# Kernel tuning notes

Measured on AMD Instinct MI355X. Metric: run time of the kernel, lower is better.

The kernel has to match this reference:

```python
import jax, jax.numpy as jnp
import numpy as np

IN_CH = 8      # in_channels
CIN = 80       # cin_channels (mel)
DI_BASE = 2
POS_GROUP = 4
NCH = 256      # n_channels
NLAYERS = 8
K = 3          # kernel_size
B = 1          # spect batch; audio batch = B * POS_GROUP
T = 4096
C2L = 2 * NCH * NLAYERS


def _conv1x1(x, w, b):
    # x: [B, C, T], w: [O, C], b: [O]
    return jnp.einsum('bct,oc->bot', x, w) + b[None, :, None]


def _dilated_conv(x, w, b, dilation):
    # x: [B, C, T], w: [O, C, K], 'same' padding as in torch Conv1d
    pad = dilation * (K - 1) // 2
    y = jax.lax.conv_general_dilated(
        x, w, window_strides=(1,), padding=[(pad, pad)],
        rhs_dilation=(dilation,), dimension_numbers=('NCH', 'OIH', 'NCH'))
    return y + b[None, :, None]


def setup_inputs() -> dict:
    key = jax.random.key(0)
    ks = jax.random.split(key, 12)
    s = 0.05
    d = {}
    d['audio'] = jax.random.normal(ks[0], (B * POS_GROUP, IN_CH, T), jnp.float32)
    d['spect'] = jax.random.normal(ks[1], (B, CIN, T), jnp.float32)
    d['pos'] = jax.random.randint(ks[2], (B * POS_GROUP,), 0, POS_GROUP)
    d['start_w'] = jax.random.normal(ks[3], (NCH, IN_CH), jnp.float32) * s
    d['start_b'] = jnp.zeros((NCH,), jnp.float32)
    d['cond_w'] = jax.random.normal(ks[4], (C2L, CIN), jnp.float32) * s
    d['cond_b'] = jnp.zeros((C2L,), jnp.float32)
    d['pos_emb_w'] = jax.random.normal(ks[5], (POS_GROUP, 128), jnp.float32) * s
    d['pos_lin_w'] = jax.random.normal(ks[6], (C2L, 128), jnp.float32) * s
    d['pos_lin_b'] = jnp.zeros((C2L,), jnp.float32)
    d['in_w'] = jax.random.normal(ks[7], (NLAYERS, 2 * NCH, NCH, K), jnp.float32) * s
    d['in_b'] = jnp.zeros((NLAYERS, 2 * NCH), jnp.float32)
    d['rs_w'] = jax.random.normal(ks[8], (NLAYERS - 1, 2 * NCH, NCH), jnp.float32) * s
    d['rs_b'] = jnp.zeros((NLAYERS - 1, 2 * NCH), jnp.float32)
    d['rs_last_w'] = jax.random.normal(ks[9], (NCH, NCH), jnp.float32) * s
    d['rs_last_b'] = jnp.zeros((NCH,), jnp.float32)
    d['end_w'] = jax.random.normal(ks[10], (2 * IN_CH, NCH), jnp.float32) * s
    d['end_b'] = jnp.zeros((2 * IN_CH,), jnp.float32)
    return d


def reference(audio, spect, pos, start_w, start_b, cond_w, cond_b,
              pos_emb_w, pos_lin_w, pos_lin_b, in_w, in_b,
              rs_w, rs_b, rs_last_w, rs_last_b, end_w, end_b):
    h = _conv1x1(audio, start_w, start_b)               # [BG, NCH, T]
    out = jnp.zeros_like(h)
    cond = _conv1x1(spect, cond_w, cond_b)              # [B, 2*NCH*L, T]
    # repeat(1, pos_group, 1).view(-1, C, T) == consecutive batch tiling
    cond = jnp.repeat(cond, POS_GROUP, axis=0)          # [BG, 2*NCH*L, T]
    pe = jax.nn.relu(pos_emb_w[pos])                    # [BG, 128]
    pc = (pe @ pos_lin_w.T + pos_lin_b)[:, :, None]     # [BG, 2*NCH*L, 1]
    for i in range(NLAYERS):
        off = i * 2 * NCH
        in_act = (_dilated_conv(h, in_w[i], in_b[i], DI_BASE ** i)
                  + cond[:, off:off + 2 * NCH]
                  + pc[:, off:off + 2 * NCH])
        acts = jnp.tanh(in_act[:, :NCH]) * jax.nn.sigmoid(in_act[:, NCH:])
        if i < NLAYERS - 1:
            rs = _conv1x1(acts, rs_w[i], rs_b[i])       # [BG, 2*NCH, T]
            h = h + rs[:, :NCH]
            out = out + rs[:, NCH:]
        else:
            out = out + _conv1x1(acts, rs_last_w, rs_last_b)
    y = _conv1x1(out, end_w, end_b)                     # [BG, 2*IN_CH, T]
    return y[:, :IN_CH], y[:, IN_CH:]
```

## Files before the change

kernel.cpp:

```cpp
#include <hip/hip_runtime.h>
#include <stdint.h>

#define T_LEN 4096
#define PAD   128
#define HROWS (T_LEN + 2*PAD)
#define NCH   256
#define M2    512
#define BG    4
#define NL    8

using f4  = __attribute__((ext_vector_type(4))) float;
using bh8 = __attribute__((ext_vector_type(8))) short;
using s4v = __attribute__((ext_vector_type(4))) short;
using u4  = __attribute__((ext_vector_type(4))) unsigned int;

static __device__ __forceinline__ short f2b(float f){
  unsigned u = __builtin_bit_cast(unsigned, f);
  unsigned r = (u + 0x7FFFu + ((u >> 16) & 1u)) >> 16;
  return (short)r;
}
static __device__ __forceinline__ float b2f(short s){
  unsigned u = ((unsigned)(unsigned short)s) << 16;
  return __builtin_bit_cast(float, u);
}

#define MFMA(a,b,c) __builtin_amdgcn_mfma_f32_16x16x32_bf16((a),(b),(c),0,0,0)


#define PAD_BLK0 1024
#define E_BLK0   1280
#define ST_BLK0  1408
#define CB_BLK0  1536
#define H0_BLK0  1600
#define ALL_BLKS 1856

__global__ __launch_bounds__(256) void prep_all(
    const float* __restrict__ audio, const float* __restrict__ spect,
    const int* __restrict__ pos, const float* __restrict__ start_w,
    const float* __restrict__ start_b, const float* __restrict__ cond_w,
    const float* __restrict__ cond_b, const float* __restrict__ pos_emb_w,
    const float* __restrict__ pos_lin_w, const float* __restrict__ pos_lin_b,
    const float* __restrict__ in_w, const float* __restrict__ in_b,
    const float* __restrict__ rs_w, const float* __restrict__ rs_b,
    const float* __restrict__ rs_last_w, const float* __restrict__ rs_last_b,
    const float* __restrict__ end_w, const float* __restrict__ end_b,
    short* __restrict__ W1, short* __restrict__ W2, short* __restrict__ Wcn,
    float* __restrict__ rsb8, short* __restrict__ hA, short* __restrict__ hB,
    short* __restrict__ Es, float* __restrict__ ebl, short* __restrict__ spectT,
    float* __restrict__ cb){
  __shared__ float smem[4224];
  const int bid = blockIdx.x, tid = threadIdx.x;

  if (bid < PAD_BLK0){
    const int G1 = NL*3*8*8*4*64;
    const int G2 = NL*8*8*2*64;
    const int G4 = NL*8*4*4*64;
    const int n3 = NL*M2;
    for (int q = bid*256 + tid; q < G1+G2+G4+n3; q += 1024*256){
      if (q < G1){
        int lane = q & 63, f = (q >> 6) & 3, kk = (q >> 8) & 7, w = (q >> 11) & 7;
        int lt = q >> 14;
        int tap = lt % 3, l = lt / 3;
        int o = (f < 2) ? (w*32 + f*16 + (lane & 15)) : (256 + w*32 + (f-2)*16 + (lane & 15));
        int c0 = kk*32 + (lane >> 4)*8;
        const float* src = in_w + (((size_t)(l*M2 + o)*NCH + c0)*3) + tap;
        bh8 pk;
        #pragma unroll
        for (int j = 0; j < 8; ++j) pk[j] = f2b(src[j*3]);
        *(bh8*)(W1 + (size_t)q*8) = pk;
      } else if (q < G1+G2){
        int p = q - G1;
        int lane = p & 63, f = (p >> 6) & 1, kk = (p >> 7) & 7, w = (p >> 10) & 7;
        int l = p >> 13;
        int o = w*32 + f*16 + (lane & 15);
        int c0 = kk*32 + (lane >> 4)*8;
        bh8 pk;
        if (l < 7){
          const f4* s = (const f4*)(rs_w + ((size_t)(l*M2 + o))*NCH + c0);
          f4 a = s[0], bvv = s[1];
          #pragma unroll
          for (int j = 0; j < 4; ++j){ pk[j] = f2b(a[j]); pk[4+j] = f2b(bvv[j]); }
        } else {
          #pragma unroll
          for (int j = 0; j < 8; ++j) pk[j] = 0;
        }
        *(bh8*)(W2 + (size_t)p*8) = pk;
      } else if (q < G1+G2+G4){
        int p = q - G1 - G2;
        int lane = p & 63, f = (p >> 6) & 3, kk = (p >> 8) & 3, w = (p >> 10) & 7;
        int l = p >> 13;
        int o = (f < 2) ? (w*32 + f*16 + (lane & 15)) : (256 + w*32 + (f-2)*16 + (lane & 15));
        int k0 = kk*32 + (lane >> 4)*8;
        bh8 pk;
        if (k0 < 80){
          const f4* s = (const f4*)(cond_w + (size_t)(l*M2 + o)*80 + k0);
          f4 a = s[0], bvv = s[1];
          #pragma unroll
          for (int j = 0; j < 4; ++j){ pk[j] = f2b(a[j]); pk[4+j] = f2b(bvv[j]); }
        } else {
          #pragma unroll
          for (int j = 0; j < 8; ++j) pk[j] = 0;
        }
        *(bh8*)(Wcn + (size_t)p*8) = pk;
      } else {
        int k = q - G1 - G2 - G4;
        int o = k & 511, l = k >> 9;
        rsb8[k] = (l < 7) ? rs_b[l*M2 + o] : 0.f;
      }
    }
  } else if (bid < E_BLK0){
    int i = (bid - PAD_BLK0)*256 + tid;
    short* h = (i < 32768) ? hA : hB;
    int j = (i & 32767) << 3;
    int b = j >> 16;
    int r = j & 65535;
    int row = r >> 8, c = r & 255;
    int grow = (row < PAD) ? row : (T_LEN + PAD + (row - PAD));
    *(u4*)(h + ((size_t)b*HROWS + grow)*NCH + c) = (u4){0,0,0,0};
  } else if (bid < ST_BLK0){
    float* ew_s = smem; float* red = smem + 256;
    int e = bid - E_BLK0;
    const int l = e >> 4, o = e & 15;
    const int c = tid;
    ew_s[c] = end_w[o*256 + c];
    __syncthreads();
    const float* Wsrc = (l < 7) ? (rs_w + ((size_t)(l*M2 + NCH))*NCH) : rs_last_w;
    float acc = 0.f;
    #pragma unroll 8
    for (int cp = 0; cp < 256; ++cp)
      acc += ew_s[cp] * Wsrc[(size_t)cp*NCH + c];
    int kk = c >> 5, g = (c >> 3) & 3, j = c & 7;
    Es[(((size_t)l*8 + kk)*64 + g*16 + o)*8 + j] = f2b(acc);
    float bv = (l < 7) ? rs_b[l*M2 + NCH + c] : rs_last_b[c];
    red[c] = ew_s[c] * bv;
    __syncthreads();
    for (int s = 128; s > 0; s >>= 1){
      if (c < s) red[c] += red[c + s];
      __syncthreads();
    }
    if (c == 0) ebl[l*16 + o] = red[0] + ((l == 0) ? end_b[o] : 0.f);
  } else if (bid < CB_BLK0){
    float (*tile)[65] = (float(*)[65])smem;
    int e = bid - ST_BLK0;
    int t0 = (e & 63)*64, k0 = (e >> 6)*64;
    for (int i = tid; i < 64*64; i += 256){
      int kr = i >> 6, tt = i & 63;
      int k = k0 + kr;
      tile[kr][tt] = (k < 80) ? spect[(size_t)k*T_LEN + t0 + tt] : 0.f;
    }
    __syncthreads();
    for (int i = tid; i < 64*64; i += 256){
      int r = i >> 6, kk = i & 63;
      spectT[(size_t)(t0 + r)*128 + k0 + kk] = f2b(tile[kk][r]);
    }
  } else if (bid < H0_BLK0){
    int e = bid - CB_BLK0;
    int b = e >> 4;
    int ch = (e & 15)*256 + tid;
    int p = pos[b];
    float acc = pos_lin_b[ch] + in_b[ch] + cond_b[ch];
    for (int k = 0; k < 128; ++k){
      float ev = pos_emb_w[p*128 + k];
      ev = ev > 0.f ? ev : 0.f;
      acc += ev * pos_lin_w[ch*128 + k];
    }
    cb[b*4096 + ch] = acc;
  } else {
    float* sw = smem; float* sb = smem + 2048;
    int e = bid - H0_BLK0;
    int b = e >> 6, t0 = (e & 63)*64;
    for (int i = tid; i < NCH*8; i += 256) sw[i] = start_w[i];
    for (int i = tid; i < NCH;   i += 256) sb[i] = start_b[i];
    __syncthreads();
    int t = t0 + (tid & 63);
    int cg = tid >> 6;
    float av[8];
    #pragma unroll
    for (int ic = 0; ic < 8; ++ic) av[ic] = audio[((size_t)(b*8 + ic))*T_LEN + t];
    short* dst = hA + ((size_t)b*HROWS + PAD + t)*NCH;
    for (int c = cg*64; c < cg*64 + 64; ++c){
      float acc = sb[c];
      #pragma unroll
      for (int ic = 0; ic < 8; ++ic) acc += sw[c*8 + ic]*av[ic];
      dst[c] = f2b(acc);
    }
  }
}

template<int DIL>
__global__ __launch_bounds__(512, 2) void wn_layer(
    const short* __restrict__ hSrc, short* __restrict__ hDst,
    const short* __restrict__ W1l, const short* __restrict__ W2l,
    const short* __restrict__ Wcl, const short* __restrict__ Esl,
    const short* __restrict__ spectTp,
    const float* __restrict__ cb_l, const float* __restrict__ rsb_l,
    const float* __restrict__ ebl_l, float* __restrict__ yacc,
    int flags){

  __shared__ short Ht[192*NCH];
  __shared__ short xb[64*NCH];
  __shared__ short St[64*128];

  constexpr int tbR   = (DIL <= 64) ? DIL : 64;
  constexpr int WROWS = (DIL <= 64) ? (64 + 2*DIL) : 192;

  const int tid  = threadIdx.x;
  const int w    = tid >> 6, lane = tid & 63;
  const int l15  = lane & 15, g = lane >> 4;
  const int lin  = blockIdx.x + (blockIdx.y << 6);
  const int nl2  = ((lin & 7) << 5) + (lin >> 3);
  const int tile = nl2 & 63, b = nl2 >> 6;
  const int sw8  = (l15 & 7) << 3;
  const bool first = flags & 1, last = flags & 2;

  f4 acc[4][4];
  #pragma unroll
  for (int f = 0; f < 4; ++f)
    #pragma unroll
    for (int nf = 0; nf < 4; ++nf) acc[f][nf] = (f4){0.f,0.f,0.f,0.f};

  bh8 Ap[3][4], Bp[3][4];

#define LAc(S, BUF) do{ const short* _p = Wcl + w*8192 + (S)*2048 + lane*8; \
    Ap[BUF][0]=*(const bh8*)(_p);      Ap[BUF][1]=*(const bh8*)(_p+512); \
    Ap[BUF][2]=*(const bh8*)(_p+1024); Ap[BUF][3]=*(const bh8*)(_p+1536); }while(0)
#define LBc(S, BUF) do{ const int _c=((S)*32+g*8)^sw8; \
    Bp[BUF][0]=*(const bh8*)(St + ( 0+l15)*128 + _c); \
    Bp[BUF][1]=*(const bh8*)(St + (16+l15)*128 + _c); \
    Bp[BUF][2]=*(const bh8*)(St + (32+l15)*128 + _c); \
    Bp[BUF][3]=*(const bh8*)(St + (48+l15)*128 + _c); }while(0)
#define LA1(S, BUF) do{ const int _tap=(S)>>3, _kk=(S)&7; \
    const short* _p = W1l + _tap*131072 + w*16384 + _kk*2048 + lane*8; \
    Ap[BUF][0]=*(const bh8*)(_p);      Ap[BUF][1]=*(const bh8*)(_p+512); \
    Ap[BUF][2]=*(const bh8*)(_p+1024); Ap[BUF][3]=*(const bh8*)(_p+1536); }while(0)
#define LB1(S, BUF) do{ const int _tap=(S)>>3, _kk=(S)&7; \
    const int _tb=_tap*tbR; const int _sw=(((_tb+l15)&7)<<3); \
    const short* _hb = Ht + (_tb+l15)*NCH + ((_kk*32+g*8)^_sw); \
    Bp[BUF][0]=*(const bh8*)(_hb); \
    Bp[BUF][1]=*(const bh8*)(_hb + 16*NCH); \
    Bp[BUF][2]=*(const bh8*)(_hb + 32*NCH); \
    Bp[BUF][3]=*(const bh8*)(_hb + 48*NCH); }while(0)
#define LAX(S, BUF) do{ if((S)<3) LAc((S),BUF); else LA1((S)-3,BUF); }while(0)
#define LBX(S, BUF) do{ if((S)<3) LBc((S),BUF); else LB1((S)-3,BUF); }while(0)
#define LA2(S, BUF) do{ \
    const short* _p = W2l + w*8192 + (S)*1024 + lane*8; \
    Ap[BUF][0]=*(const bh8*)(_p);      Ap[BUF][1]=*(const bh8*)(_p+512); }while(0)
#define LB2(S, BUF) do{ const int _c=((S)*32+g*8)^sw8; \
    Bp[BUF][0]=*(const bh8*)(xb + ( 0+l15)*NCH + _c); \
    Bp[BUF][1]=*(const bh8*)(xb + (16+l15)*NCH + _c); \
    Bp[BUF][2]=*(const bh8*)(xb + (32+l15)*NCH + _c); \
    Bp[BUF][3]=*(const bh8*)(xb + (48+l15)*NCH + _c); }while(0)

  LAX(0, 0);

  {
    constexpr int SEGS = WROWS/2;
    #pragma unroll
    for (int k = 0; k < (SEGS + 7)/8; ++k){
      int seg = w + k*8;
      if (SEGS % 8 == 0 || seg < SEGS){
        int r = seg*2 + (lane >> 5);
        int grow = (DIL <= 64) ? (tile*64 - DIL + r)
                               : (tile*64 + ((r >> 6) - 1)*128 + (r & 63));
        int cb = ((lane & 31) << 4) ^ ((r & 7) << 4);
        const short* gp = hSrc + ((size_t)(b*HROWS + PAD + grow))*NCH + (cb >> 1);
        __builtin_amdgcn_global_load_lds(
            (const __attribute__((address_space(1))) unsigned int*)gp,
            (__attribute__((address_space(3))) unsigned int*)(Ht + seg*512),
            16, 0, 0);
      }
    }
    #pragma unroll
    for (int k = 0; k < 2; ++k){
      int seg = w + k*8;
      int r = seg*4 + (lane >> 4);
      int cb = ((lane & 15) << 4) ^ ((r & 7) << 4);
      const short* gp = spectTp + (size_t)(tile*64 + r)*128 + (cb >> 1);
      __builtin_amdgcn_global_load_lds(
          (const __attribute__((address_space(1))) unsigned int*)gp,
          (__attribute__((address_space(3))) unsigned int*)(St + seg*512),
          16, 0, 0);
    }
  }
  LAX(1, 1);
  __syncthreads();

  LBX(0, 0);
  LBX(1, 1);
  #pragma unroll
  for (int s = 0; s < 27; ++s){
    const int cur = s % 3, pf = (s+2) % 3;
    if (s < 25){ LAX(s+2, pf); LBX(s+2, pf); }
    #pragma unroll
    for (int f = 0; f < 4; ++f)
      #pragma unroll
      for (int nf = 0; nf < 4; ++nf)
        acc[f][nf] = MFMA(Ap[cur][f], Bp[cur][nf], acc[f][nf]);
  }

  float bias[4][4];
  #pragma unroll
  for (int f = 0; f < 4; ++f){
    int ch = ((f < 2) ? (w*32 + f*16) : (256 + w*32 + (f-2)*16)) + 4*g;
    f4 t = *(const f4*)(cb_l + b*4096 + ch);
    #pragma unroll
    for (int j = 0; j < 4; ++j) bias[f][j] = t[j];
  }
  float rbv[2][4];
  #pragma unroll
  for (int f = 0; f < 2; ++f){
    f4 t = *(const f4*)(rsb_l + w*32 + f*16 + 4*g);
    #pragma unroll
    for (int j = 0; j < 4; ++j) rbv[f][j] = t[j];
  }

  #pragma unroll
  for (int f = 0; f < 2; ++f){
    #pragma unroll
    for (int nf = 0; nf < 4; ++nf){
      int tl = nf*16 + l15;
      s4v pk;
      #pragma unroll
      for (int j = 0; j < 4; ++j){
        float xl = acc[f][nf][j]   + bias[f][j];
        float xh = acc[f+2][nf][j] + bias[f+2][j];
        xl = fminf(fmaxf(xl, -30.f), 30.f);
        xh = fminf(fmaxf(xh, -30.f), 30.f);
        float e2 = __expf(2.f*xl);
        float th = (e2 - 1.f)/(e2 + 1.f);
        float sg = 1.f/(1.f + __expf(-xh));
        pk[j] = f2b(th * sg);
      }
      *(s4v*)(xb + tl*NCH + ((w*32 + f*16 + 4*g) ^ sw8)) = pk;
    }
  }
  if (!last) LA2(0, 0);
  __syncthreads();

  if (!last){
    #pragma unroll
    for (int f = 0; f < 2; ++f)
      #pragma unroll
      for (int nf = 0; nf < 4; ++nf) acc[f][nf] = (f4){0.f,0.f,0.f,0.f};
    LB2(0, 0);
    #pragma unroll
    for (int s = 0; s < 8; ++s){
      const int cur = s & 1, nxt = cur ^ 1;
      if (s < 7){ LA2(s+1, nxt); LB2(s+1, nxt); }
      #pragma unroll
      for (int f = 0; f < 2; ++f)
        #pragma unroll
        for (int nf = 0; nf < 4; ++nf)
          acc[f][nf] = MFMA(Ap[cur][f], Bp[cur][nf], acc[f][nf]);
    }
    constexpr int swcBase = tbR & 7;
    const int swc = (((swcBase + l15) & 7) << 3);
    #pragma unroll
    for (int f = 0; f < 2; ++f){
      #pragma unroll
      for (int nf = 0; nf < 4; ++nf){
        int tl = nf*16 + l15;
        int cb0 = w*32 + f*16 + 4*g;
        s4v hold = *(const s4v*)(Ht + (tbR + tl)*NCH + (cb0 ^ swc));
        s4v pk;
        #pragma unroll
        for (int j = 0; j < 4; ++j)
          pk[j] = f2b(b2f(hold[j]) + acc[f][nf][j] + rbv[f][j]);
        *(s4v*)(hDst + ((size_t)b*HROWS + PAD + tile*64 + tl)*NCH + cb0) = pk;
      }
    }
  }
  {
    const int nfq = w & 3, kh = w >> 2;
    f4 ya = (f4){0.f,0.f,0.f,0.f};
    #pragma unroll
    for (int s = 0; s < 4; ++s){
      int kks = kh*4 + s;
      bh8 av = *(const bh8*)(Esl + ((size_t)kks*64 + lane)*8);
      bh8 bv = *(const bh8*)(xb + (nfq*16 + l15)*NCH + ((kks*32 + g*8) ^ sw8));
      ya = MFMA(av, bv, ya);
    }
    float* yp = yacc + (((size_t)(b*T_LEN + tile*64 + nfq*16 + l15))*2 + kh)*16 + g*4;
    f4 prev = first ? (f4){0.f,0.f,0.f,0.f} : *(const f4*)yp;
    f4 o;
    #pragma unroll
    for (int j = 0; j < 4; ++j)
      o[j] = prev[j] + ya[j] + ((kh == 0) ? ebl_l[g*4 + j] : 0.f);
    *(f4*)yp = o;
  }
#undef LAc
#undef LBc
#undef LA1
#undef LB1
#undef LAX
#undef LBX
#undef LA2
#undef LB2
}

__global__ void final_y(const float* __restrict__ yacc, float* __restrict__ y){
  __shared__ float tl[16][65];
  int b = blockIdx.y, t0 = blockIdx.x*64;
  int i = threadIdx.x;
  #pragma unroll
  for (int s = 0; s < 4; ++s){
    int idx = i + s*256;
    int t = idx >> 4, o = idx & 15;
    size_t base = ((size_t)(b*T_LEN + t0 + t))*32 + o;
    tl[o][t] = yacc[base] + yacc[base + 16];
  }
  __syncthreads();
  #pragma unroll
  for (int s = 0; s < 4; ++s){
    int idx = i + s*256;
    int o = idx >> 6, t = idx & 63;
    float v = tl[o][t];
    float* dst = (o < 8) ? (y + ((size_t)(b*8 + o))*T_LEN)
                         : (y + 131072 + ((size_t)(b*8 + o - 8))*T_LEN);
    dst[t0 + t] = v;
  }
}

extern "C" void kernel_launch(void* const* d_in, const int* in_sizes, int n_in,
                              void* d_out, int out_size, void* d_ws, size_t ws_size,
                              hipStream_t stream){
  const float* audio      = (const float*)d_in[0];
  const float* spect      = (const float*)d_in[1];
  const int*   pos        = (const int*)  d_in[2];
  const float* start_w    = (const float*)d_in[3];
  const float* start_b    = (const float*)d_in[4];
  const float* cond_w     = (const float*)d_in[5];
  const float* cond_b     = (const float*)d_in[6];
  const float* pos_emb_w  = (const float*)d_in[7];
  const float* pos_lin_w  = (const float*)d_in[8];
  const float* pos_lin_b  = (const float*)d_in[9];
  const float* in_w       = (const float*)d_in[10];
  const float* in_b       = (const float*)d_in[11];
  const float* rs_w       = (const float*)d_in[12];
  const float* rs_b       = (const float*)d_in[13];
  const float* rs_last_w  = (const float*)d_in[14];
  const float* rs_last_b  = (const float*)d_in[15];
  const float* end_w      = (const float*)d_in[16];
  const float* end_b      = (const float*)d_in[17];
  float* y = (float*)d_out;

  char* ws = (char*)d_ws;
  size_t off = 0;
  auto alloc = [&](size_t bytes) -> void* {
    void* p = ws + off;
    off += (bytes + 255) & ~(size_t)255;
    return p;
  };
  const size_t hBytes = (size_t)BG*HROWS*NCH*2;
  short* hA     = (short*)alloc(hBytes);
  short* hB     = (short*)alloc(hBytes);
  short* W1     = (short*)alloc((size_t)NL*3*8*8*4*512*2);
  short* W2     = (short*)alloc((size_t)NL*8*8*2*512*2);
  short* Wcn    = (short*)alloc((size_t)NL*8*4*4*512*2);
  float* rsb8   = (float*)alloc((size_t)NL*M2*4);
  float* cb     = (float*)alloc((size_t)BG*4096*4);
  short* spectT = (short*)alloc((size_t)4096*128*2);
  short* Es     = (short*)alloc((size_t)NL*8*64*8*2);
  float* ebl    = (float*)alloc((size_t)NL*16*4);
  float* yacc   = (float*)alloc((size_t)BG*T_LEN*2*16*4);
  if (off > ws_size) return;

  prep_all<<<ALL_BLKS, 256, 0, stream>>>(
      audio, spect, pos, start_w, start_b, cond_w, cond_b, pos_emb_w, pos_lin_w,
      pos_lin_b, in_w, in_b, rs_w, rs_b, rs_last_w, rs_last_b, end_w, end_b,
      W1, W2, Wcn, rsb8, hA, hB, Es, ebl, spectT, cb);

  for (int l = 0; l < NL; ++l){
    const short* hS = (l & 1) ? hB : hA;
    short*       hD = (l & 1) ? hA : hB;
    int flags = (l == 0 ? 1 : 0) | (l == NL-1 ? 2 : 0);
    const short* W1p = W1 + (size_t)l*3*131072;
    const short* W2p = W2 + (size_t)l*65536;
    const short* Wcp = Wcn + (size_t)l*65536;
    const short* Esp = Es + (size_t)l*4096;
    const float* cbp = cb + l*M2;
    const float* rbp = rsb8 + l*M2;
    const float* ebp = ebl + l*16;
    dim3 grid(64, BG);
    switch (l){
      case 0: wn_layer<  1><<<grid, 512, 0, stream>>>(hS, hD, W1p, W2p, Wcp, Esp, spectT, cbp, rbp, ebp, yacc, flags); break;
      case 1: wn_layer<  2><<<grid, 512, 0, stream>>>(hS, hD, W1p, W2p, Wcp, Esp, spectT, cbp, rbp, ebp, yacc, flags); break;
      case 2: wn_layer<  4><<<grid, 512, 0, stream>>>(hS, hD, W1p, W2p, Wcp, Esp, spectT, cbp, rbp, ebp, yacc, flags); break;
      case 3: wn_layer<  8><<<grid, 512, 0, stream>>>(hS, hD, W1p, W2p, Wcp, Esp, spectT, cbp, rbp, ebp, yacc, flags); break;
      case 4: wn_layer< 16><<<grid, 512, 0, stream>>>(hS, hD, W1p, W2p, Wcp, Esp, spectT, cbp, rbp, ebp, yacc, flags); break;
      case 5: wn_layer< 32><<<grid, 512, 0, stream>>>(hS, hD, W1p, W2p, Wcp, Esp, spectT, cbp, rbp, ebp, yacc, flags); break;
      case 6: wn_layer< 64><<<grid, 512, 0, stream>>>(hS, hD, W1p, W2p, Wcp, Esp, spectT, cbp, rbp, ebp, yacc, flags); break;
      case 7: wn_layer<128><<<grid, 512, 0, stream>>>(hS, hD, W1p, W2p, Wcp, Esp, spectT, cbp, rbp, ebp, yacc, flags); break;
    }
  }
  final_y<<<dim3(64, BG), 256, 0, stream>>>(yacc, y);
}
```

Before: 230.1 us.

## Halve time tile to 32 per block, doubling grid and raising occupancy

Shrinks the per-block time tile from 64 to 32 samples, so each layer launches 512 blocks instead of 256. Per-wave accumulators and B fragments are halved, LDS sized to the tile, and launch bounds raised to allow 4 blocks per CU. The end-projection partial sums are split across four k-quarters instead of two, with the yacc buffer and final reduction widened to match. The aim is better CU fill and latency hiding, at the cost of reloading the full weight matrices twice as often per time step and a larger halo overhead relative to the tile.

After: 268.0 us. +16.5%, slower.

```diff
diff --git a/kernel.cpp b/kernel.cpp
--- a/kernel.cpp
+++ b/kernel.cpp
@@ -188,7 +188,7 @@
 }
 
 template<int DIL>
-__global__ __launch_bounds__(512, 2) void wn_layer(
+__global__ __launch_bounds__(512, 4) void wn_layer(
     const short* __restrict__ hSrc, short* __restrict__ hDst,
     const short* __restrict__ W1l, const short* __restrict__ W2l,
     const short* __restrict__ Wcl, const short* __restrict__ Esl,
@@ -197,38 +197,37 @@
     const float* __restrict__ ebl_l, float* __restrict__ yacc,
     int flags){
 
-  __shared__ short Ht[192*NCH];
-  __shared__ short xb[64*NCH];
-  __shared__ short St[64*128];
-
-  constexpr int tbR   = (DIL <= 64) ? DIL : 64;
-  constexpr int WROWS = (DIL <= 64) ? (64 + 2*DIL) : 192;
+  constexpr int TT    = 32;
+  constexpr int tbR   = (DIL <= TT) ? DIL : TT;
+  constexpr int WROWS = (DIL <= TT) ? (TT + 2*DIL) : 3*TT;
+
+  __shared__ short Ht[WROWS*NCH];
+  __shared__ short xb[TT*NCH];
+  __shared__ short St[TT*128];
 
   const int tid  = threadIdx.x;
   const int w    = tid >> 6, lane = tid & 63;
   const int l15  = lane & 15, g = lane >> 4;
-  const int lin  = blockIdx.x + (blockIdx.y << 6);
-  const int nl2  = ((lin & 7) << 5) + (lin >> 3);
-  const int tile = nl2 & 63, b = nl2 >> 6;
+  const int lin  = blockIdx.x + (blockIdx.y << 7);
+  const int nl2  = ((lin & 7) << 6) + (lin >> 3);
+  const int tile = nl2 & 127, b = nl2 >> 7;
   const int sw8  = (l15 & 7) << 3;
   const bool first = flags & 1, last = flags & 2;
 
-  f4 acc[4][4];
+  f4 acc[4][2];
   #pragma unroll
   for (int f = 0; f < 4; ++f)
     #pragma unroll
-    for (int nf = 0; nf < 4; ++nf) acc[f][nf] = (f4){0.f,0.f,0.f,0.f};
-
-  bh8 Ap[3][4], Bp[3][4];
+    for (int nf = 0; nf < 2; ++nf) acc[f][nf] = (f4){0.f,0.f,0.f,0.f};
+
+  bh8 Ap[3][4], Bp[3][2];
 
 #define LAc(S, BUF) do{ const short* _p = Wcl + w*8192 + (S)*2048 + lane*8; \
     Ap[BUF][0]=*(const bh8*)(_p);      Ap[BUF][1]=*(const bh8*)(_p+512); \
     Ap[BUF][2]=*(const bh8*)(_p+1024); Ap[BUF][3]=*(const bh8*)(_p+1536); }while(0)
 #define LBc(S, BUF) do{ const int _c=((S)*32+g*8)^sw8; \
     Bp[BUF][0]=*(const bh8*)(St + ( 0+l15)*128 + _c); \
-    Bp[BUF][1]=*(const bh8*)(St + (16+l15)*128 + _c); \
-    Bp[BUF][2]=*(const bh8*)(St + (32+l15)*128 + _c); \
-    Bp[BUF][3]=*(const bh8*)(St + (48+l15)*128 + _c); }while(0)
+    Bp[BUF][1]=*(const bh8*)(St + (16+l15)*128 + _c); }while(0)
 #define LA1(S, BUF) do{ const int _tap=(S)>>3, _kk=(S)&7; \
     const short* _p = W1l + _tap*131072 + w*16384 + _kk*2048 + lane*8; \
     Ap[BUF][0]=*(const bh8*)(_p);      Ap[BUF][1]=*(const bh8*)(_p+512); \
@@ -237,9 +236,7 @@
     const int _tb=_tap*tbR; const int _sw=(((_tb+l15)&7)<<3); \
     const short* _hb = Ht + (_tb+l15)*NCH + ((_kk*32+g*8)^_sw); \
     Bp[BUF][0]=*(const bh8*)(_hb); \
-    Bp[BUF][1]=*(const bh8*)(_hb + 16*NCH); \
-    Bp[BUF][2]=*(const bh8*)(_hb + 32*NCH); \
-    Bp[BUF][3]=*(const bh8*)(_hb + 48*NCH); }while(0)
+    Bp[BUF][1]=*(const bh8*)(_hb + 16*NCH); }while(0)
 #define LAX(S, BUF) do{ if((S)<3) LAc((S),BUF); else LA1((S)-3,BUF); }while(0)
 #define LBX(S, BUF) do{ if((S)<3) LBc((S),BUF); else LB1((S)-3,BUF); }while(0)
 #define LA2(S, BUF) do{ \
@@ -247,9 +244,7 @@
     Ap[BUF][0]=*(const bh8*)(_p);      Ap[BUF][1]=*(const bh8*)(_p+512); }while(0)
 #define LB2(S, BUF) do{ const int _c=((S)*32+g*8)^sw8; \
     Bp[BUF][0]=*(const bh8*)(xb + ( 0+l15)*NCH + _c); \
-    Bp[BUF][1]=*(const bh8*)(xb + (16+l15)*NCH + _c); \
-    Bp[BUF][2]=*(const bh8*)(xb + (32+l15)*NCH + _c); \
-    Bp[BUF][3]=*(const bh8*)(xb + (48+l15)*NCH + _c); }while(0)
+    Bp[BUF][1]=*(const bh8*)(xb + (16+l15)*NCH + _c); }while(0)
 
   LAX(0, 0);
 
@@ -260,8 +255,8 @@
       int seg = w + k*8;
       if (SEGS % 8 == 0 || seg < SEGS){
         int r = seg*2 + (lane >> 5);
-        int grow = (DIL <= 64) ? (tile*64 - DIL + r)
-                               : (tile*64 + ((r >> 6) - 1)*128 + (r & 63));
+        int grow = (DIL <= TT) ? (tile*TT - DIL + r)
+                               : (tile*TT + ((r >> 5) - 1)*DIL + (r & 31));
         int cb = ((lane & 31) << 4) ^ ((r & 7) << 4);
         const short* gp = hSrc + ((size_t)(b*HROWS + PAD + grow))*NCH + (cb >> 1);
         __builtin_amdgcn_global_load_lds(
@@ -270,12 +265,11 @@
             16, 0, 0);
       }
     }
-    #pragma unroll
-    for (int k = 0; k < 2; ++k){
-      int seg = w + k*8;
+    {
+      int seg = w;
       int r = seg*4 + (lane >> 4);
       int cb = ((lane & 15) << 4) ^ ((r & 7) << 4);
-      const short* gp = spectTp + (size_t)(tile*64 + r)*128 + (cb >> 1);
+      const short* gp = spectTp + (size_t)(tile*TT + r)*128 + (cb >> 1);
       __builtin_amdgcn_global_load_lds(
           (const __attribute__((address_space(1))) unsigned int*)gp,
           (__attribute__((address_space(3))) unsigned int*)(St + seg*512),
@@ -294,7 +288,7 @@
     #pragma unroll
     for (int f = 0; f < 4; ++f)
       #pragma unroll
-      for (int nf = 0; nf < 4; ++nf)
+      for (int nf = 0; nf < 2; ++nf)
         acc[f][nf] = MFMA(Ap[cur][f], Bp[cur][nf], acc[f][nf]);
   }
 
@@ -317,7 +311,7 @@
   #pragma unroll
   for (int f = 0; f < 2; ++f){
     #pragma unroll
-    for (int nf = 0; nf < 4; ++nf){
+    for (int nf = 0; nf < 2; ++nf){
       int tl = nf*16 + l15;
       s4v pk;
       #pragma unroll
@@ -341,7 +335,7 @@
     #pragma unroll
     for (int f = 0; f < 2; ++f)
       #pragma unroll
-      for (int nf = 0; nf < 4; ++nf) acc[f][nf] = (f4){0.f,0.f,0.f,0.f};
+      for (int nf = 0; nf < 2; ++nf) acc[f][nf] = (f4){0.f,0.f,0.f,0.f};
     LB2(0, 0);
     #pragma unroll
     for (int s = 0; s < 8; ++s){
@@ -350,7 +344,7 @@
       #pragma unroll
       for (int f = 0; f < 2; ++f)
         #pragma unroll
-        for (int nf = 0; nf < 4; ++nf)
+        for (int nf = 0; nf < 2; ++nf)
           acc[f][nf] = MFMA(Ap[cur][f], Bp[cur][nf], acc[f][nf]);
     }
     constexpr int swcBase = tbR & 7;
@@ -358,7 +352,7 @@
     #pragma unroll
     for (int f = 0; f < 2; ++f){
       #pragma unroll
-      for (int nf = 0; nf < 4; ++nf){
+      for (int nf = 0; nf < 2; ++nf){
         int tl = nf*16 + l15;
         int cb0 = w*32 + f*16 + 4*g;
         s4v hold = *(const s4v*)(Ht + (tbR + tl)*NCH + (cb0 ^ swc));
@@ -366,26 +360,26 @@
         #pragma unroll
         for (int j = 0; j < 4; ++j)
           pk[j] = f2b(b2f(hold[j]) + acc[f][nf][j] + rbv[f][j]);
-        *(s4v*)(hDst + ((size_t)b*HROWS + PAD + tile*64 + tl)*NCH + cb0) = pk;
+        *(s4v*)(hDst + ((size_t)b*HROWS + PAD + tile*TT + tl)*NCH + cb0) = pk;
       }
     }
   }
   {
-    const int nfq = w & 3, kh = w >> 2;
+    const int th = w & 1, kq = w >> 1;
     f4 ya = (f4){0.f,0.f,0.f,0.f};
     #pragma unroll
-    for (int s = 0; s < 4; ++s){
-      int kks = kh*4 + s;
+    for (int s = 0; s < 2; ++s){
+      int kks = kq*2 + s;
       bh8 av = *(const bh8*)(Esl + ((size_t)kks*64 + lane)*8);
-      bh8 bv = *(const bh8*)(xb + (nfq*16 + l15)*NCH + ((kks*32 + g*8) ^ sw8));
+      bh8 bv = *(const bh8*)(xb + (th*16 + l15)*NCH + ((kks*32 + g*8) ^ sw8));
       ya = MFMA(av, bv, ya);
     }
-    float* yp = yacc + (((size_t)(b*T_LEN + tile*64 + nfq*16 + l15))*2 + kh)*16 + g*4;
+    float* yp = yacc + (((size_t)(b*T_LEN + tile*TT + th*16 + l15))*4 + kq)*16 + g*4;
     f4 prev = first ? (f4){0.f,0.f,0.f,0.f} : *(const f4*)yp;
     f4 o;
     #pragma unroll
     for (int j = 0; j < 4; ++j)
-      o[j] = prev[j] + ya[j] + ((kh == 0) ? ebl_l[g*4 + j] : 0.f);
+      o[j] = prev[j] + ya[j] + ((kq == 0) ? ebl_l[g*4 + j] : 0.f);
     *(f4*)yp = o;
   }
 #undef LAc
@@ -406,8 +400,8 @@
   for (int s = 0; s < 4; ++s){
     int idx = i + s*256;
     int t = idx >> 4, o = idx & 15;
-    size_t base = ((size_t)(b*T_LEN + t0 + t))*32 + o;
-    tl[o][t] = yacc[base] + yacc[base + 16];
+    size_t base = ((size_t)(b*T_LEN + t0 + t))*64 + o;
+    tl[o][t] = yacc[base] + yacc[base + 16] + yacc[base + 32] + yacc[base + 48];
   }
   __syncthreads();
   #pragma unroll
@@ -462,7 +456,7 @@
   short* spectT = (short*)alloc((size_t)4096*128*2);
   short* Es     = (short*)alloc((size_t)NL*8*64*8*2);
   float* ebl    = (float*)alloc((size_t)NL*16*4);
-  float* yacc   = (float*)alloc((size_t)BG*T_LEN*2*16*4);
+  float* yacc   = (float*)alloc((size_t)BG*T_LEN*4*16*4);
   if (off > ws_size) return;
 
   prep_all<<<ALL_BLKS, 256, 0, stream>>>(
@@ -481,7 +475,7 @@
     const float* cbp = cb + l*M2;
     const float* rbp = rsb8 + l*M2;
     const float* ebp = ebl + l*16;
-    dim3 grid(64, BG);
+    dim3 grid(128, BG);
     switch (l){
       case 0: wn_layer<  1><<<grid, 512, 0, stream>>>(hS, hD, W1p, W2p, Wcp, Esp, spectT, cbp, rbp, ebp, yacc, flags); break;
       case 1: wn_layer<  2><<<grid, 512, 0, stream>>>(hS, hD, W1p, W2p, Wcp, Esp, spectT, cbp, rbp, ebp, yacc, flags); break;
```
